# Optimization experiments

Measured on AMD Instinct MI355X. Metric: run time of the kernel, lower is better.

The kernel has to match this reference:

```python
import jax, jax.numpy as jnp
import numpy as np

EPS = 1e-6
NUM_HEADS = 16  # config.num_attention_heads

def _rms(h, w):
    h32 = h.astype(jnp.float32)
    v = jnp.mean(h32 * h32, axis=-1, keepdims=True)
    return (w * h32 * jax.lax.rsqrt(v + EPS)).astype(h.dtype)

def _rope(q, k, pos):
    dh = q.shape[-1]
    inv = 1.0 / (10000.0 ** (jnp.arange(0, dh, 2, dtype=jnp.float32) / dh))
    ang = pos.astype(jnp.float32)[:, None] * inv[None, :]  # [n, dh/2]
    cos = jnp.concatenate([jnp.cos(ang), jnp.cos(ang)], -1)[None, None]  # [1,1,n,dh]
    sin = jnp.concatenate([jnp.sin(ang), jnp.sin(ang)], -1)[None, None]
    def rot(x):
        x1, x2 = x[..., :dh // 2], x[..., dh // 2:]
        return jnp.concatenate([-x2, x1], -1)
    return q * cos + rot(q) * sin, k * cos + rot(k) * sin

def _skip_causal_mask(N, block_size, len1, text_len):
    qi = jnp.arange(N)[:, None]
    ki = jnp.arange(N)[None, :]
    qb = (qi - text_len) // block_size
    kb = (ki - text_len) // block_size
    iq = qi >= text_len
    ik = ki >= text_len
    return (((ki < text_len) & (qi >= ki))
            | (iq & ik & (qb < len1) & (kb < len1) & (qb >= kb))
            | (iq & ik & (qb >= len1) & (kb < len1) & (qb - len1 > kb))
            | (iq & ik & (qb == kb)))

def _layer(x, position_ids, text_position_ids, qkv_w, qkv_b, proj_w, proj_b,
           qn_w, kn_w, ln1_w, ln2_w, gate_w, up_w, down_w,
           block_size, text_len, len1):
    B, N, C = x.shape
    H = NUM_HEADS
    Dh = C // H
    T = text_len
    Lc = len1 * block_size
    offs = [0, T, T + Lc]
    lens = [T, Lc, N - T - Lc]  # text / clean / noised segment lengths
    qs, ks, vs = [], [], []
    for i in range(3):
        seg = _rms(x[:, offs[i]:offs[i] + lens[i]], ln1_w[i])  # input layernorm
        qkv = seg @ qkv_w[i] + qkv_b[i]                        # [B,n,3C]
        qkv = qkv.reshape(B, lens[i], 3, H, Dh).transpose(2, 0, 3, 1, 4)
        qs.append(_rms(qkv[0], qn_w[i]))
        ks.append(_rms(qkv[1], kn_w[i]))
        vs.append(qkv[2])
    img_q = jnp.concatenate([qs[1], qs[2]], axis=2)
    img_k = jnp.concatenate([ks[1], ks[2]], axis=2)
    img_q, img_k = _rope(img_q, img_k, position_ids)
    txt_q, txt_k = _rope(qs[0], ks[0], text_position_ids)
    q = jnp.concatenate([txt_q, img_q], axis=2)
    k = jnp.concatenate([txt_k, img_k], axis=2)
    v = jnp.concatenate(vs, axis=2)
    scores = jnp.einsum('bhqd,bhkd->bhqk', q, k) / np.float32(np.sqrt(Dh))
    mask = _skip_causal_mask(N, block_size, len1, text_len)
    scores = jnp.where(mask, scores, jnp.finfo(scores.dtype).min)
    attn = jax.nn.softmax(scores, axis=-1)
    o = jnp.einsum('bhqk,bhkd->bhqd', attn, v)
    o = o.transpose(0, 2, 1, 3).reshape(B, N, C)
    o = jnp.concatenate([o[:, offs[i]:offs[i] + lens[i]] @ proj_w[i] + proj_b[i]
                         for i in range(3)], axis=1)
    h = x + o
    mlp = []
    for i in range(3):
        y = _rms(h[:, offs[i]:offs[i] + lens[i]], ln2_w[i])  # post-attn layernorm
        mlp.append((jax.nn.silu(y @ gate_w[i]) * (y @ up_w[i])) @ down_w[i])
    return h + jnp.concatenate(mlp, axis=1)

def setup_inputs():
    key = jax.random.key(0)
    ks = jax.random.split(key, 8)
    B, C, H, I = 2, 1024, 16, 4096
    block_size, text_len, len1, len2 = 128, 256, 4, 4
    N = text_len + (len1 + len2) * block_size  # 1280
    s = 0.02
    return {
        'x': jax.random.normal(ks[0], (B, N, C), jnp.float32),
        'position_ids': jnp.arange((len1 + len2) * block_size, dtype=jnp.int32),
        'text_position_ids': jnp.arange(text_len, dtype=jnp.int32),
        'qkv_w': jax.random.normal(ks[1], (3, C, 3 * C), jnp.float32) * s,
        'qkv_b': jnp.zeros((3, 3 * C), jnp.float32),
        'proj_w': jax.random.normal(ks[2], (3, C, C), jnp.float32) * s,
        'proj_b': jnp.zeros((3, C), jnp.float32),
        'qn_w': jnp.ones((3, C // H), jnp.float32),
        'kn_w': jnp.ones((3, C // H), jnp.float32),
        'ln1_w': jnp.ones((3, C), jnp.float32),
        'ln2_w': jnp.ones((3, C), jnp.float32),
        'gate_w': jax.random.normal(ks[3], (3, C, I), jnp.float32) * s,
        'up_w': jax.random.normal(ks[4], (3, C, I), jnp.float32) * s,
        'down_w': jax.random.normal(ks[5], (3, I, C), jnp.float32) * s,
        'block_size': block_size, 'text_len': text_len, 'len1': len1,
    }

def reference(x, position_ids, text_position_ids, qkv_w, qkv_b, proj_w, proj_b,
              qn_w, kn_w, ln1_w, ln2_w, gate_w, up_w, down_w,
              block_size, text_len, len1):
    return _layer(x, position_ids, text_position_ids, qkv_w, qkv_b, proj_w, proj_b,
                  qn_w, kn_w, ln1_w, ln2_w, gate_w, up_w, down_w,
                  block_size, text_len, len1)
```

## Files before the change

kernel.cpp:

```cpp
#include <hip/hip_runtime.h>
#include <math.h>

constexpr int Bb  = 2;
constexpr int Nn  = 1280;
constexpr int Cc  = 1024;
constexpr int Hh  = 16;
constexpr int DH  = 64;
constexpr int Ii  = 4096;
constexpr int Tt  = 256;
constexpr int BSz = 128;
constexpr int L1  = 4;
constexpr int Mrows = Bb * Nn;

typedef __attribute__((ext_vector_type(8))) short short8v;
typedef __attribute__((ext_vector_type(4))) float f32x4;

__device__ __forceinline__ int segof(int n) {
    return n < Tt ? 0 : (n < Tt + L1 * BSz ? 1 : 2);
}
__device__ __forceinline__ unsigned short f2bf(float f) {
    unsigned int u = __float_as_uint(f);
    u += 0x7fffu + ((u >> 16) & 1u);
    return (unsigned short)(u >> 16);
}
__device__ __forceinline__ float bf2f(unsigned short h) {
    return __uint_as_float(((unsigned int)h) << 16);
}

__device__ __forceinline__ int xcd_swz(int lin, int nwg) {
    int cpx = nwg >> 3;
    return (lin & 7) * cpx + (lin >> 3);
}

__global__ __launch_bounds__(256)
void rms_bf16(const float* __restrict__ in, const float* __restrict__ w,
              unsigned short* __restrict__ out) {
    int row = blockIdx.x;
    int n   = row % Nn;
    int seg = segof(n);
    const float* x = in + (size_t)row * Cc;
    int t = threadIdx.x;
    float4 xv = reinterpret_cast<const float4*>(x)[t];
    float ss = xv.x * xv.x + xv.y * xv.y + xv.z * xv.z + xv.w * xv.w;
#pragma unroll
    for (int off = 32; off; off >>= 1) ss += __shfl_down(ss, off, 64);
    __shared__ float red[4];
    __shared__ float s_r;
    int lane = t & 63, wid = t >> 6;
    if (lane == 0) red[wid] = ss;
    __syncthreads();
    if (t == 0) s_r = rsqrtf((red[0] + red[1] + red[2] + red[3]) * (1.0f / Cc) + 1e-6f);
    __syncthreads();
    float r = s_r;
    float4 wv = reinterpret_cast<const float4*>(w + (size_t)seg * Cc)[t];
    ushort4 ov;
    ov.x = f2bf(wv.x * xv.x * r);
    ov.y = f2bf(wv.y * xv.y * r);
    ov.z = f2bf(wv.z * xv.z * r);
    ov.w = f2bf(wv.w * xv.w * r);
    *reinterpret_cast<ushort4*>(&out[(size_t)row * Cc + t * 4]) = ov;
}

__global__ __launch_bounds__(256)
void pack_w(const float* __restrict__ W, unsigned short* __restrict__ PB,
            int K, int Nd) {
    size_t idx = (size_t)blockIdx.x * 256 + threadIdx.x;
    size_t cpseg = (size_t)K * Nd / 8;
    int s = (int)(idx / cpseg);
    size_t rm = idx % cpseg;
    int lane = (int)(rm & 63);
    int fr   = (int)((rm >> 6) & 7);
    size_t tile = rm >> 9;
    int nct = Nd >> 7;
    int cb = (int)(tile % nct);
    int kt = (int)(tile / nct);
    int col = cb * 128 + fr * 16 + (lane & 15);
    int k0  = kt * 32 + (lane >> 4) * 8;
    const float* src = W + ((size_t)s * K + k0) * Nd + col;
    unsigned short o[8];
#pragma unroll
    for (int j = 0; j < 8; j++) o[j] = f2bf(src[(size_t)j * Nd]);
    short8v v;
#pragma unroll
    for (int j = 0; j < 8; j++) v[j] = (short)o[j];
    *reinterpret_cast<short8v*>(&PB[idx * 8]) = v;
}

template <int OUTMODE, bool BIAS, int NZ>
__global__ __launch_bounds__(256)
void gemm64(const unsigned short* __restrict__ A,
            const unsigned short* __restrict__ PB,
            const float* __restrict__ bias, void* __restrict__ outp,
            int K, int Nd) {
    __shared__ __align__(16) unsigned short lds[12288];
    int bx = blockIdx.x, by = blockIdx.y, bz = (NZ > 1) ? blockIdx.z : 0;
    {
        int gx = gridDim.x, gy = gridDim.y, gz = (NZ > 1) ? gridDim.z : 1;
        int lin = bx + gx * (by + gy * bz);
        int swz = xcd_swz(lin, gx * gy * gz);
        bx = swz % gx; swz /= gx;
        by = swz % gy; bz = swz / gy;
    }
    int rb = bx * 64, cb = by;
    int seg = segof(rb % Nn);
    int tid = threadIdx.x, lane = tid & 63, wid = tid >> 6;
    int wr = wid >> 1, wc = wid & 1;
    int g = lane >> 4, c_ = lane & 15;
    const unsigned short* PBseg = PB + (size_t)seg * K * Nd;
    const int nct = Nd >> 7;
    const int Keff = K / NZ;
    const int nKt = Keff >> 6;
    const int kz = bz * Keff;

    f32x4 acc[2][4];
#pragma unroll
    for (int m = 0; m < 2; m++)
#pragma unroll
        for (int n = 0; n < 4; n++) acc[m][n] = (f32x4){0.f, 0.f, 0.f, 0.f};

    short8v av[2], bv[4];
    auto load_tile = [&](int kt) {
#pragma unroll
        for (int i = 0; i < 2; i++) {
            int c = tid + i * 256;
            int rf = c >> 7, kb = (c >> 6) & 1, lc = c & 63;
            int row = rb + rf * 16 + (lc & 15);
            int k0  = kz + kt * 64 + kb * 32 + (lc >> 4) * 8;
            av[i] = *reinterpret_cast<const short8v*>(&A[(size_t)row * K + k0]);
        }
#pragma unroll
        for (int i = 0; i < 4; i++) {
            int c = tid + i * 256;
            int cf = c >> 7, kb = (c >> 6) & 1, lc = c & 63;
            int kt32 = (kz >> 5) + kt * 2 + kb;
            bv[i] = *reinterpret_cast<const short8v*>(
                &PBseg[((((size_t)kt32 * nct + cb) * 8 + cf) * 64 + lc) * 8]);
        }
    };

    load_tile(0);
    for (int kt = 0; kt < nKt; ++kt) {
        __syncthreads();
#pragma unroll
        for (int i = 0; i < 2; i++)
            *reinterpret_cast<short8v*>(&lds[(size_t)(tid + i * 256) * 8]) = av[i];
#pragma unroll
        for (int i = 0; i < 4; i++)
            *reinterpret_cast<short8v*>(&lds[4096 + (size_t)(tid + i * 256) * 8]) = bv[i];
        __syncthreads();
        if (kt + 1 < nKt) load_tile(kt + 1);
        short8v afr[2][2], bfr[4][2];
#pragma unroll
        for (int m = 0; m < 2; m++)
#pragma unroll
            for (int kb = 0; kb < 2; kb++)
                afr[m][kb] = *reinterpret_cast<short8v*>(
                    &lds[(((wr * 2 + m) * 2 + kb) * 64 + lane) * 8]);
#pragma unroll
        for (int n = 0; n < 4; n++)
#pragma unroll
            for (int kb = 0; kb < 2; kb++)
                bfr[n][kb] = *reinterpret_cast<short8v*>(
                    &lds[4096 + (((wc * 4 + n) * 2 + kb) * 64 + lane) * 8]);
#pragma unroll
        for (int m = 0; m < 2; m++)
#pragma unroll
            for (int n = 0; n < 4; n++)
#pragma unroll
                for (int kb = 0; kb < 2; kb++)
                    acc[m][n] = __builtin_amdgcn_mfma_f32_16x16x32_bf16(
                        afr[m][kb], bfr[n][kb], acc[m][n], 0, 0, 0);
    }

    float* outf = (float*)outp;
    unsigned short* outh = (unsigned short*)outp;
    size_t zoff = (NZ > 1) ? (size_t)bz * Mrows * Nd : 0;
#pragma unroll
    for (int n = 0; n < 4; n++) {
        int col = cb * 128 + wc * 64 + n * 16 + c_;
        float bvv = BIAS ? bias[(size_t)seg * Nd + col] : 0.f;
#pragma unroll
        for (int m = 0; m < 2; m++) {
#pragma unroll
            for (int r = 0; r < 4; r++) {
                int row = rb + wr * 32 + m * 16 + g * 4 + r;
                float v = acc[m][n][r] + bvv;
                if (OUTMODE == 0) outf[zoff + (size_t)row * Nd + col] = v;
                else              outh[zoff + (size_t)row * Nd + col] = f2bf(v);
            }
        }
    }
}

__global__ __launch_bounds__(256)
void gemm_gu(const unsigned short* __restrict__ A,
             const unsigned short* __restrict__ PG,
             const unsigned short* __restrict__ PU,
             unsigned short* __restrict__ outp) {
    __shared__ __align__(16) unsigned short lds[10240];
    int bx = blockIdx.x, by = blockIdx.y;
    {
        int lin = bx + gridDim.x * by;
        int swz = xcd_swz(lin, gridDim.x * gridDim.y);
        bx = swz % gridDim.x; by = swz / gridDim.x;
    }
    int rb = bx * 64, cb = by;
    int seg = segof(rb % Nn);
    int tid = threadIdx.x, lane = tid & 63, wid = tid >> 6;
    int wr = wid >> 1, wc = wid & 1;
    int g = lane >> 4, c_ = lane & 15;
    const int nct = Ii >> 7;
    const unsigned short* PGseg = PG + (size_t)seg * Cc * Ii;
    const unsigned short* PUseg = PU + (size_t)seg * Cc * Ii;

    f32x4 accG[2][4], accU[2][4];
#pragma unroll
    for (int m = 0; m < 2; m++)
#pragma unroll
        for (int n = 0; n < 4; n++) {
            accG[m][n] = (f32x4){0.f, 0.f, 0.f, 0.f};
            accU[m][n] = (f32x4){0.f, 0.f, 0.f, 0.f};
        }

    int mf0 = tid >> 6, lc0 = tid & 63;
    const unsigned short* gA =
        &A[(size_t)(rb + mf0 * 16 + (lc0 & 15)) * Cc + (lc0 >> 4) * 8];
    const size_t bstep = (size_t)nct * 4096;
    short8v av, gv[2], uv[2];
    auto load_tile = [&](int kt) {
        av = *reinterpret_cast<const short8v*>(gA + kt * 32);
#pragma unroll
        for (int i = 0; i < 2; i++) {
            int c = tid + i * 256;
            int cf = c >> 6, lc = c & 63;
            size_t off = (((size_t)kt * nct + cb) * 8 + cf) * 64 * 8 + (size_t)lc * 8;
            gv[i] = *reinterpret_cast<const short8v*>(PGseg + off);
            uv[i] = *reinterpret_cast<const short8v*>(PUseg + off);
        }
    };

    const int nKt = Cc >> 5;
    load_tile(0);
    for (int kt = 0; kt < nKt; ++kt) {
        __syncthreads();
        *reinterpret_cast<short8v*>(&lds[(size_t)tid * 8]) = av;
#pragma unroll
        for (int i = 0; i < 2; i++) {
            *reinterpret_cast<short8v*>(&lds[2048 + (size_t)(tid + i * 256) * 8]) = gv[i];
            *reinterpret_cast<short8v*>(&lds[6144 + (size_t)(tid + i * 256) * 8]) = uv[i];
        }
        __syncthreads();
        if (kt + 1 < nKt) load_tile(kt + 1);
        short8v afr[2], gfr[4], ufr[4];
#pragma unroll
        for (int m = 0; m < 2; m++)
            afr[m] = *reinterpret_cast<short8v*>(&lds[((wr * 2 + m) * 64 + lane) * 8]);
#pragma unroll
        for (int n = 0; n < 4; n++) {
            gfr[n] = *reinterpret_cast<short8v*>(&lds[2048 + ((wc * 4 + n) * 64 + lane) * 8]);
            ufr[n] = *reinterpret_cast<short8v*>(&lds[6144 + ((wc * 4 + n) * 64 + lane) * 8]);
        }
#pragma unroll
        for (int m = 0; m < 2; m++)
#pragma unroll
            for (int n = 0; n < 4; n++) {
                accG[m][n] = __builtin_amdgcn_mfma_f32_16x16x32_bf16(
                    afr[m], gfr[n], accG[m][n], 0, 0, 0);
                accU[m][n] = __builtin_amdgcn_mfma_f32_16x16x32_bf16(
                    afr[m], ufr[n], accU[m][n], 0, 0, 0);
            }
    }

#pragma unroll
    for (int n = 0; n < 4; n++) {
        int col = cb * 128 + wc * 64 + n * 16 + c_;
#pragma unroll
        for (int m = 0; m < 2; m++) {
#pragma unroll
            for (int r = 0; r < 4; r++) {
                int row = rb + wr * 32 + m * 16 + g * 4 + r;
                float gval = accG[m][n][r], uval = accU[m][n][r];
                float t = gval / (1.f + __expf(-gval)) * uval;
                outp[(size_t)row * Ii + col] = f2bf(t);
            }
        }
    }
}

__global__ __launch_bounds__(256)
void combine_proj(const float* __restrict__ x, const float* __restrict__ bias,
                  const float* __restrict__ p, float* __restrict__ hb) {
    int i = blockIdx.x * 256 + threadIdx.x;
    int base = i * 4;
    int col = base % Cc;
    int n   = (base / Cc) % Nn;
    int seg = segof(n);
    float4 a = reinterpret_cast<const float4*>(x)[i];
    float4 b = *reinterpret_cast<const float4*>(&bias[(size_t)seg * Cc + col]);
    float4 p0 = reinterpret_cast<const float4*>(p)[i];
    float4 p1 = reinterpret_cast<const float4*>(p)[i + Mrows * Cc / 4];
    float4 r;
    r.x = a.x + b.x + p0.x + p1.x;
    r.y = a.y + b.y + p0.y + p1.y;
    r.z = a.z + b.z + p0.z + p1.z;
    r.w = a.w + b.w + p0.w + p1.w;
    reinterpret_cast<float4*>(hb)[i] = r;
}

__global__ __launch_bounds__(256)
void combine_down4(const unsigned short* __restrict__ p,
                   float* __restrict__ out) {
    int i = blockIdx.x * 256 + threadIdx.x;
    float4 a = reinterpret_cast<const float4*>(out)[i];
#pragma unroll
    for (int z = 0; z < 4; z++) {
        ushort4 u = *reinterpret_cast<const ushort4*>(&p[(size_t)z * Mrows * Cc + i * 4]);
        a.x += bf2f(u.x); a.y += bf2f(u.y); a.z += bf2f(u.z); a.w += bf2f(u.w);
    }
    reinterpret_cast<float4*>(out)[i] = a;
}

__global__ __launch_bounds__(256)
void split_rope(const unsigned short* __restrict__ qkv,
                const float* __restrict__ qn_w, const float* __restrict__ kn_w,
                const int* __restrict__ pos_ids, const int* __restrict__ tpos_ids,
                unsigned short* __restrict__ Q, unsigned short* __restrict__ K,
                unsigned short* __restrict__ V) {
    int row = blockIdx.x;
    int b = row / Nn, n = row % Nn;
    int seg = segof(n);
    int lane = threadIdx.x & 63, wid = threadIdx.x >> 6;
    int pos = (n < Tt) ? tpos_ids[n] : pos_ids[n - Tt];
    int j = lane & 31;
    float ang = (float)pos * exp2f(-(float)j * (13.287712379549449f / 32.f));
    float cv = cosf(ang), sv = sinf(ang);
    float qw = qn_w[seg * DH + lane], kw = kn_w[seg * DH + lane];
    for (int h = wid; h < Hh; h += 4) {
        const unsigned short* base = qkv + (size_t)row * (3 * Cc) + h * DH + lane;
        float q = bf2f(base[0]), k = bf2f(base[Cc]), v = bf2f(base[2 * Cc]);
        float qs = q * q, ks = k * k;
#pragma unroll
        for (int off = 32; off; off >>= 1) {
            qs += __shfl_xor(qs, off, 64);
            ks += __shfl_xor(ks, off, 64);
        }
        q = q * rsqrtf(qs * (1.f / DH) + 1e-6f) * qw;
        k = k * rsqrtf(ks * (1.f / DH) + 1e-6f) * kw;
        float qp = __shfl_xor(q, 32, 64);
        float kp = __shfl_xor(k, 32, 64);
        float qo = q * cv + ((lane < 32) ? -qp * sv : qp * sv);
        float ko = k * cv + ((lane < 32) ? -kp * sv : kp * sv);
        size_t oidx = ((size_t)(b * Hh + h) * Nn + n) * DH + lane;
        Q[oidx] = f2bf(qo);
        K[oidx] = f2bf(ko);
        V[oidx] = f2bf(v);
    }
}

__global__ __launch_bounds__(256)
void attn_mfma(const unsigned short* __restrict__ Qg,
               const unsigned short* __restrict__ Kg,
               const unsigned short* __restrict__ Vg,
               unsigned short* __restrict__ O) {
    __shared__ __align__(16) unsigned short k_lds[64 * 64];
    __shared__ __align__(16) unsigned short vt_lds[64 * 64];
    __shared__ __align__(16) unsigned short p_lds[4][16 * 64];

    int qt = blockIdx.x;
    int bh = blockIdx.y;
    int b = bh >> 4, h = bh & 15;
    int tid = threadIdx.x, lane = tid & 63, wid = tid >> 6;
    int g = lane >> 4, c = lane & 15;

    const size_t headoff = (size_t)bh * Nn * DH;
    int q0 = qt * 64;
    bool qtext = q0 < Tt;
    int qb = qtext ? 0 : (q0 - Tt) / BSz;

    int qrow_frag = q0 + wid * 16 + c;
    short8v aq[2];
#pragma unroll
    for (int kb = 0; kb < 2; kb++)
        aq[kb] = *reinterpret_cast<const short8v*>(
            &Qg[headoff + (size_t)qrow_frag * DH + kb * 32 + g * 8]);

    unsigned short* pbuf = &p_lds[wid][0];

    f32x4 o_[4];
#pragma unroll
    for (int nb = 0; nb < 4; nb++) o_[nb] = (f32x4){0.f, 0.f, 0.f, 0.f};
    float m_[4] = {-3.4e38f, -3.4e38f, -3.4e38f, -3.4e38f};
    float l_[4] = {0.f, 0.f, 0.f, 0.f};

    int tr = tid >> 2, tc = tid & 3;

    for (int kt = 0; kt < Nn / 64; kt++) {
        int kbase = kt * 64;
        bool vis, diag = false;
        if (qtext) {
            vis = (kbase <= q0);
            diag = (kbase == q0);
        } else if (kbase < Tt) {
            vis = true;
        } else {
            int kb = (kbase - Tt) / BSz;
            vis = (qb < L1) ? (kb <= qb)
                            : ((kb < L1 && qb - L1 > kb) || kb == qb);
        }
        if (!vis) continue;

        __syncthreads();
        {
            const unsigned short* ks = &Kg[headoff + (size_t)(kbase + tr) * DH];
            const unsigned short* vs = &Vg[headoff + (size_t)(kbase + tr) * DH];
#pragma unroll
            for (int i = 0; i < 2; i++) {
                int ch = tc + i * 4;
                short8v kv = *reinterpret_cast<const short8v*>(ks + ch * 8);
                int byte = (tr * 128 + ch * 16) ^ ((tr & 7) << 4);
                *reinterpret_cast<short8v*>((char*)k_lds + byte) = kv;
                short8v vv = *reinterpret_cast<const short8v*>(vs + ch * 8);
#pragma unroll
                for (int j = 0; j < 8; j++) {
                    int dh = ch * 8 + j;
                    int vbyte = (dh * 128 + tr * 2) ^ ((dh & 7) << 4);
                    *reinterpret_cast<unsigned short*>((char*)vt_lds + vbyte) =
                        (unsigned short)vv[j];
                }
            }
        }
        __syncthreads();

        f32x4 s_[4];
#pragma unroll
        for (int nb = 0; nb < 4; nb++) s_[nb] = (f32x4){0.f, 0.f, 0.f, 0.f};
#pragma unroll
        for (int nb = 0; nb < 4; nb++) {
            int kil = nb * 16 + c;
#pragma unroll
            for (int kb = 0; kb < 2; kb++) {
                int byte = (kil * 128 + kb * 64 + g * 16) ^ ((kil & 7) << 4);
                short8v bk = *reinterpret_cast<short8v*>((char*)k_lds + byte);
                s_[nb] = __builtin_amdgcn_mfma_f32_16x16x32_bf16(aq[kb], bk, s_[nb], 0, 0, 0);
            }
        }
#pragma unroll
        for (int nb = 0; nb < 4; nb++) {
#pragma unroll
            for (int r = 0; r < 4; r++) {
                float sv = s_[nb][r] * 0.125f;
                if (diag) {
                    int qrl = wid * 16 + g * 4 + r;
                    int kcl = nb * 16 + c;
                    if (qrl < kcl) sv = -3.4e38f;
                }
                s_[nb][r] = sv;
            }
        }
#pragma unroll
        for (int r = 0; r < 4; r++) {
            float mx = fmaxf(fmaxf(s_[0][r], s_[1][r]), fmaxf(s_[2][r], s_[3][r]));
#pragma unroll
            for (int off = 1; off <= 8; off <<= 1)
                mx = fmaxf(mx, __shfl_xor(mx, off, 64));
            float mn = fmaxf(m_[r], mx);
            float es = __expf(m_[r] - mn);
            m_[r] = mn;
            float pv[4];
            float rs = 0.f;
#pragma unroll
            for (int nb = 0; nb < 4; nb++) {
                pv[nb] = __expf(s_[nb][r] - mn);
                rs += pv[nb];
            }
#pragma unroll
            for (int off = 1; off <= 8; off <<= 1)
                rs += __shfl_xor(rs, off, 64);
            l_[r] = l_[r] * es + rs;
#pragma unroll
            for (int nb = 0; nb < 4; nb++) o_[nb][r] *= es;
            int qrl = g * 4 + r;
            int swz = (qrl & 7) << 4;
#pragma unroll
            for (int nb = 0; nb < 4; nb++) {
                int byte = (qrl * 128 + (nb * 16 + c) * 2) ^ swz;
                *reinterpret_cast<unsigned short*>((char*)pbuf + byte) = f2bf(pv[nb]);
            }
        }
        short8v aP[2];
#pragma unroll
        for (int kb = 0; kb < 2; kb++) {
            int byte = (c * 128 + kb * 64 + g * 16) ^ ((c & 7) << 4);
            aP[kb] = *reinterpret_cast<short8v*>((char*)pbuf + byte);
        }
#pragma unroll
        for (int nb = 0; nb < 4; nb++) {
            int dh = nb * 16 + c;
#pragma unroll
            for (int kb = 0; kb < 2; kb++) {
                int byte = (dh * 128 + kb * 64 + g * 16) ^ ((dh & 7) << 4);
                short8v bv = *reinterpret_cast<short8v*>((char*)vt_lds + byte);
                o_[nb] = __builtin_amdgcn_mfma_f32_16x16x32_bf16(aP[kb], bv, o_[nb], 0, 0, 0);
            }
        }
    }

    float inv_[4];
#pragma unroll
    for (int r = 0; r < 4; r++) inv_[r] = 1.f / l_[r];
#pragma unroll
    for (int nb = 0; nb < 4; nb++) {
        int col = h * DH + nb * 16 + c;
#pragma unroll
        for (int r = 0; r < 4; r++) {
            int row = q0 + wid * 16 + g * 4 + r;
            O[((size_t)b * Nn + row) * Cc + col] = f2bf(o_[nb][r] * inv_[r]);
        }
    }
}

extern "C" void kernel_launch(void* const* d_in, const int* in_sizes, int n_in,
                              void* d_out, int out_size, void* d_ws, size_t ws_size,
                              hipStream_t stream) {
    const float* x        = (const float*)d_in[0];
    const int*   pos_ids  = (const int*)d_in[1];
    const int*   tpos_ids = (const int*)d_in[2];
    const float* qkv_w    = (const float*)d_in[3];
    const float* qkv_b    = (const float*)d_in[4];
    const float* proj_w   = (const float*)d_in[5];
    const float* proj_b   = (const float*)d_in[6];
    const float* qn_w     = (const float*)d_in[7];
    const float* kn_w     = (const float*)d_in[8];
    const float* ln1_w    = (const float*)d_in[9];
    const float* ln2_w    = (const float*)d_in[10];
    const float* gate_w   = (const float*)d_in[11];
    const float* up_w     = (const float*)d_in[12];
    const float* down_w   = (const float*)d_in[13];
    float* out = (float*)d_out;
    char*  wsb = (char*)d_ws;

    unsigned short* WA  = (unsigned short*)(wsb);
    unsigned short* WB  = (unsigned short*)(wsb + 25165824);
    unsigned short* Tb  = (unsigned short*)(wsb + 50331648);
    unsigned short* P3  = (unsigned short*)(wsb + 71303168);
    unsigned short* Qbf = Tb;
    unsigned short* Kbf = Tb + 2621440;
    unsigned short* Vbf = Tb + 5242880;

    rms_bf16<<<Mrows, 256, 0, stream>>>(x, ln1_w, P3);
    pack_w<<<4608, 256, 0, stream>>>(qkv_w, WA, Cc, 3 * Cc);
    gemm64<1, true, 1><<<dim3(Mrows / 64, 24), 256, 0, stream>>>(
        P3, WA, qkv_b, WB, Cc, 3 * Cc);
    split_rope<<<Mrows, 256, 0, stream>>>(WB, qn_w, kn_w, pos_ids, tpos_ids,
                                          Qbf, Kbf, Vbf);
    attn_mfma<<<dim3(Nn / 64, Bb * Hh), 256, 0, stream>>>(Qbf, Kbf, Vbf, P3);
    pack_w<<<1536, 256, 0, stream>>>(proj_w, WA, Cc, Cc);
    gemm64<0, false, 2><<<dim3(Mrows / 64, 8, 2), 256, 0, stream>>>(
        P3, WA, nullptr, (float*)Tb, Cc, Cc);
    combine_proj<<<Mrows * Cc / 1024, 256, 0, stream>>>(x, proj_b, (float*)Tb, out);
    rms_bf16<<<Mrows, 256, 0, stream>>>(out, ln2_w, P3);
    pack_w<<<6144, 256, 0, stream>>>(gate_w, WA, Cc, Ii);
    pack_w<<<6144, 256, 0, stream>>>(up_w, WB, Cc, Ii);
    gemm_gu<<<dim3(Mrows / 64, 32), 256, 0, stream>>>(P3, WA, WB, Tb);
    pack_w<<<6144, 256, 0, stream>>>(down_w, WA, Ii, Cc);
    gemm64<1, false, 4><<<dim3(Mrows / 64, 8, 4), 256, 0, stream>>>(
        Tb, WA, nullptr, WB, Ii, Cc);
    combine_down4<<<Mrows * Cc / 1024, 256, 0, stream>>>(WB, out);
}
```

Before: 287.1 us.

## Enlarge GEMM block tiles to 128x128 with 32-wide K steps

Measured after the change: 275.2 us. 4.1% less time.

```diff
diff --git a/kernel.cpp b/kernel.cpp
--- a/kernel.cpp
+++ b/kernel.cpp
@@ -87,12 +87,12 @@
 }
 
 template <int OUTMODE, bool BIAS, int NZ>
-__global__ __launch_bounds__(256)
-void gemm64(const unsigned short* __restrict__ A,
-            const unsigned short* __restrict__ PB,
-            const float* __restrict__ bias, void* __restrict__ outp,
-            int K, int Nd) {
-    __shared__ __align__(16) unsigned short lds[12288];
+__global__ __launch_bounds__(256, 2)
+void gemm128r(const unsigned short* __restrict__ A,
+              const unsigned short* __restrict__ PB,
+              const float* __restrict__ bias, void* __restrict__ outp,
+              int K, int Nd) {
+    __shared__ __align__(16) unsigned short lds[8192];
     int bx = blockIdx.x, by = blockIdx.y, bz = (NZ > 1) ? blockIdx.z : 0;
     {
         int gx = gridDim.x, gy = gridDim.y, gz = (NZ > 1) ? gridDim.z : 1;
@@ -101,75 +101,66 @@
         bx = swz % gx; swz /= gx;
         by = swz % gy; bz = swz / gy;
     }
-    int rb = bx * 64, cb = by;
+    int rb = bx * 128, cb = by;
     int seg = segof(rb % Nn);
     int tid = threadIdx.x, lane = tid & 63, wid = tid >> 6;
     int wr = wid >> 1, wc = wid & 1;
     int g = lane >> 4, c_ = lane & 15;
-    const unsigned short* PBseg = PB + (size_t)seg * K * Nd;
     const int nct = Nd >> 7;
     const int Keff = K / NZ;
-    const int nKt = Keff >> 6;
+    const int nKt = Keff >> 5;
     const int kz = bz * Keff;
-
-    f32x4 acc[2][4];
-#pragma unroll
-    for (int m = 0; m < 2; m++)
+    const unsigned short* PBseg = PB + (size_t)seg * K * Nd;
+
+    int mf0 = tid >> 6, lc0 = tid & 63;
+    const unsigned short* pA0 =
+        A + (size_t)(rb + mf0 * 16 + (lc0 & 15)) * K + kz + (lc0 >> 4) * 8;
+    const unsigned short* pA1 = pA0 + (size_t)64 * K;
+    const unsigned short* pB0 =
+        PBseg + (((size_t)(kz >> 5) * nct + cb) * 8 + mf0) * 512 + (size_t)lc0 * 8;
+    const unsigned short* pB1 = pB0 + 2048;
+    const size_t bstep = (size_t)nct * 4096;
+
+    f32x4 acc[4][4];
+#pragma unroll
+    for (int m = 0; m < 4; m++)
 #pragma unroll
         for (int n = 0; n < 4; n++) acc[m][n] = (f32x4){0.f, 0.f, 0.f, 0.f};
 
-    short8v av[2], bv[4];
-    auto load_tile = [&](int kt) {
-#pragma unroll
-        for (int i = 0; i < 2; i++) {
-            int c = tid + i * 256;
-            int rf = c >> 7, kb = (c >> 6) & 1, lc = c & 63;
-            int row = rb + rf * 16 + (lc & 15);
-            int k0  = kz + kt * 64 + kb * 32 + (lc >> 4) * 8;
-            av[i] = *reinterpret_cast<const short8v*>(&A[(size_t)row * K + k0]);
-        }
-#pragma unroll
-        for (int i = 0; i < 4; i++) {
-            int c = tid + i * 256;
-            int cf = c >> 7, kb = (c >> 6) & 1, lc = c & 63;
-            int kt32 = (kz >> 5) + kt * 2 + kb;
-            bv[i] = *reinterpret_cast<const short8v*>(
-                &PBseg[((((size_t)kt32 * nct + cb) * 8 + cf) * 64 + lc) * 8]);
-        }
-    };
-
-    load_tile(0);
+    short8v av[2], bv[2];
+    av[0] = *reinterpret_cast<const short8v*>(pA0);
+    av[1] = *reinterpret_cast<const short8v*>(pA1);
+    bv[0] = *reinterpret_cast<const short8v*>(pB0);
+    bv[1] = *reinterpret_cast<const short8v*>(pB1);
+    pA0 += 32; pA1 += 32; pB0 += bstep; pB1 += bstep;
+
     for (int kt = 0; kt < nKt; ++kt) {
         __syncthreads();
-#pragma unroll
-        for (int i = 0; i < 2; i++)
-            *reinterpret_cast<short8v*>(&lds[(size_t)(tid + i * 256) * 8]) = av[i];
-#pragma unroll
-        for (int i = 0; i < 4; i++)
-            *reinterpret_cast<short8v*>(&lds[4096 + (size_t)(tid + i * 256) * 8]) = bv[i];
+        *reinterpret_cast<short8v*>(&lds[(size_t)tid * 8]) = av[0];
+        *reinterpret_cast<short8v*>(&lds[(size_t)(tid + 256) * 8]) = av[1];
+        *reinterpret_cast<short8v*>(&lds[4096 + (size_t)tid * 8]) = bv[0];
+        *reinterpret_cast<short8v*>(&lds[4096 + (size_t)(tid + 256) * 8]) = bv[1];
         __syncthreads();
-        if (kt + 1 < nKt) load_tile(kt + 1);
-        short8v afr[2][2], bfr[4][2];
-#pragma unroll
-        for (int m = 0; m < 2; m++)
-#pragma unroll
-            for (int kb = 0; kb < 2; kb++)
-                afr[m][kb] = *reinterpret_cast<short8v*>(
-                    &lds[(((wr * 2 + m) * 2 + kb) * 64 + lane) * 8]);
+        if (kt + 1 < nKt) {
+            av[0] = *reinterpret_cast<const short8v*>(pA0);
+            av[1] = *reinterpret_cast<const short8v*>(pA1);
+            bv[0] = *reinterpret_cast<const short8v*>(pB0);
+            bv[1] = *reinterpret_cast<const short8v*>(pB1);
+            pA0 += 32; pA1 += 32; pB0 += bstep; pB1 += bstep;
+        }
+        short8v afr[4], bfr[4];
+#pragma unroll
+        for (int m = 0; m < 4; m++)
+            afr[m] = *reinterpret_cast<short8v*>(&lds[((wr * 4 + m) * 64 + lane) * 8]);
 #pragma unroll
         for (int n = 0; n < 4; n++)
-#pragma unroll
-            for (int kb = 0; kb < 2; kb++)
-                bfr[n][kb] = *reinterpret_cast<short8v*>(
-                    &lds[4096 + (((wc * 4 + n) * 2 + kb) * 64 + lane) * 8]);
-#pragma unroll
-        for (int m = 0; m < 2; m++)
+            bfr[n] = *reinterpret_cast<short8v*>(&lds[4096 + ((wc * 4 + n) * 64 + lane) * 8]);
+#pragma unroll
+        for (int m = 0; m < 4; m++)
 #pragma unroll
             for (int n = 0; n < 4; n++)
-#pragma unroll
-                for (int kb = 0; kb < 2; kb++)
-                    acc[m][n] = __builtin_amdgcn_mfma_f32_16x16x32_bf16(
-                        afr[m][kb], bfr[n][kb], acc[m][n], 0, 0, 0);
+                acc[m][n] = __builtin_amdgcn_mfma_f32_16x16x32_bf16(
+                    afr[m], bfr[n], acc[m][n], 0, 0, 0);
     }
 
     float* outf = (float*)outp;
@@ -180,10 +171,10 @@
         int col = cb * 128 + wc * 64 + n * 16 + c_;
         float bvv = BIAS ? bias[(size_t)seg * Nd + col] : 0.f;
 #pragma unroll
-        for (int m = 0; m < 2; m++) {
+        for (int m = 0; m < 4; m++) {
 #pragma unroll
             for (int r = 0; r < 4; r++) {
-                int row = rb + wr * 32 + m * 16 + g * 4 + r;
+                int row = rb + wr * 64 + m * 16 + g * 4 + r;
                 float v = acc[m][n][r] + bvv;
                 if (OUTMODE == 0) outf[zoff + (size_t)row * Nd + col] = v;
                 else              outh[zoff + (size_t)row * Nd + col] = f2bf(v);
@@ -192,19 +183,19 @@
     }
 }
 
-__global__ __launch_bounds__(256)
+__global__ __launch_bounds__(256, 2)
 void gemm_gu(const unsigned short* __restrict__ A,
              const unsigned short* __restrict__ PG,
              const unsigned short* __restrict__ PU,
              unsigned short* __restrict__ outp) {
-    __shared__ __align__(16) unsigned short lds[10240];
+    __shared__ __align__(16) unsigned short lds[12288];
     int bx = blockIdx.x, by = blockIdx.y;
     {
         int lin = bx + gridDim.x * by;
         int swz = xcd_swz(lin, gridDim.x * gridDim.y);
         bx = swz % gridDim.x; by = swz / gridDim.x;
     }
-    int rb = bx * 64, cb = by;
+    int rb = bx * 128, cb = by;
     int seg = segof(rb % Nn);
     int tid = threadIdx.x, lane = tid & 63, wid = tid >> 6;
     int wr = wid >> 1, wc = wid & 1;
@@ -213,72 +204,92 @@
     const unsigned short* PGseg = PG + (size_t)seg * Cc * Ii;
     const unsigned short* PUseg = PU + (size_t)seg * Cc * Ii;
 
-    f32x4 accG[2][4], accU[2][4];
-#pragma unroll
-    for (int m = 0; m < 2; m++)
+    int mf0 = tid >> 6, lc0 = tid & 63;
+    const unsigned short* pA0 =
+        A + (size_t)(rb + mf0 * 16 + (lc0 & 15)) * Cc + (lc0 >> 4) * 8;
+    const unsigned short* pA1 = pA0 + (size_t)64 * Cc;
+    size_t boff = ((size_t)cb * 8 + mf0) * 512 + (size_t)lc0 * 8;
+    const unsigned short* pG0 = PGseg + boff;
+    const unsigned short* pG1 = pG0 + 2048;
+    const unsigned short* pU0 = PUseg + boff;
+    const unsigned short* pU1 = pU0 + 2048;
+    const size_t bstep = (size_t)nct * 4096;
+
+    f32x4 accG[4][4], accU[4][4];
+#pragma unroll
+    for (int m = 0; m < 4; m++)
 #pragma unroll
         for (int n = 0; n < 4; n++) {
             accG[m][n] = (f32x4){0.f, 0.f, 0.f, 0.f};
             accU[m][n] = (f32x4){0.f, 0.f, 0.f, 0.f};
         }
 
-    int mf0 = tid >> 6, lc0 = tid & 63;
-    const unsigned short* gA =
-        &A[(size_t)(rb + mf0 * 16 + (lc0 & 15)) * Cc + (lc0 >> 4) * 8];
-    const size_t bstep = (size_t)nct * 4096;
-    short8v av, gv[2], uv[2];
-    auto load_tile = [&](int kt) {
-        av = *reinterpret_cast<const short8v*>(gA + kt * 32);
-#pragma unroll
-        for (int i = 0; i < 2; i++) {
-            int c = tid + i * 256;
-            int cf = c >> 6, lc = c & 63;
-            size_t off = (((size_t)kt * nct + cb) * 8 + cf) * 64 * 8 + (size_t)lc * 8;
-            gv[i] = *reinterpret_cast<const short8v*>(PGseg + off);
-            uv[i] = *reinterpret_cast<const short8v*>(PUseg + off);
-        }
-    };
+    short8v av[2], gv[2], uv[2];
+    av[0] = *reinterpret_cast<const short8v*>(pA0);
+    av[1] = *reinterpret_cast<const short8v*>(pA1);
+    gv[0] = *reinterpret_cast<const short8v*>(pG0);
+    gv[1] = *reinterpret_cast<const short8v*>(pG1);
+    uv[0] = *reinterpret_cast<const short8v*>(pU0);
+    uv[1] = *reinterpret_cast<const short8v*>(pU1);
+    pA0 += 32; pA1 += 32; pG0 += bstep; pG1 += bstep; pU0 += bstep; pU1 += bstep;
 
     const int nKt = Cc >> 5;
-    load_tile(0);
     for (int kt = 0; kt < nKt; ++kt) {
         __syncthreads();
-        *reinterpret_cast<short8v*>(&lds[(size_t)tid * 8]) = av;
-#pragma unroll
-        for (int i = 0; i < 2; i++) {
-            *reinterpret_cast<short8v*>(&lds[2048 + (size_t)(tid + i * 256) * 8]) = gv[i];
-            *reinterpret_cast<short8v*>(&lds[6144 + (size_t)(tid + i * 256) * 8]) = uv[i];
-        }
+        *reinterpret_cast<short8v*>(&lds[(size_t)tid * 8]) = av[0];
+        *reinterpret_cast<short8v*>(&lds[(size_t)(tid + 256) * 8]) = av[1];
+        *reinterpret_cast<short8v*>(&lds[4096 + (size_t)tid * 8]) = gv[0];
+        *reinterpret_cast<short8v*>(&lds[4096 + (size_t)(tid + 256) * 8]) = gv[1];
+        *reinterpret_cast<short8v*>(&lds[8192 + (size_t)tid * 8]) = uv[0];
+        *reinterpret_cast<short8v*>(&lds[8192 + (size_t)(tid + 256) * 8]) = uv[1];
         __syncthreads();
-        if (kt + 1 < nKt) load_tile(kt + 1);
-        short8v afr[2], gfr[4], ufr[4];
-#pragma unroll
-        for (int m = 0; m < 2; m++)
-            afr[m] = *reinterpret_cast<short8v*>(&lds[((wr * 2 + m) * 64 + lane) * 8]);
-#pragma unroll
-        for (int n = 0; n < 4; n++) {
-            gfr[n] = *reinterpret_cast<short8v*>(&lds[2048 + ((wc * 4 + n) * 64 + lane) * 8]);
-            ufr[n] = *reinterpret_cast<short8v*>(&lds[6144 + ((wc * 4 + n) * 64 + lane) * 8]);
-        }
-#pragma unroll
-        for (int m = 0; m < 2; m++)
-#pragma unroll
-            for (int n = 0; n < 4; n++) {
-                accG[m][n] = __builtin_amdgcn_mfma_f32_16x16x32_bf16(
-                    afr[m], gfr[n], accG[m][n], 0, 0, 0);
-                accU[m][n] = __builtin_amdgcn_mfma_f32_16x16x32_bf16(
-                    afr[m], ufr[n], accU[m][n], 0, 0, 0);
-            }
+        if (kt + 1 < nKt) {
+            av[0] = *reinterpret_cast<const short8v*>(pA0);
+            av[1] = *reinterpret_cast<const short8v*>(pA1);
+            gv[0] = *reinterpret_cast<const short8v*>(pG0);
+            gv[1] = *reinterpret_cast<const short8v*>(pG1);
+            uv[0] = *reinterpret_cast<const short8v*>(pU0);
+            uv[1] = *reinterpret_cast<const short8v*>(pU1);
+            pA0 += 32; pA1 += 32; pG0 += bstep; pG1 += bstep; pU0 += bstep; pU1 += bstep;
+        }
+        short8v afr[4];
+#pragma unroll
+        for (int m = 0; m < 4; m++)
+            afr[m] = *reinterpret_cast<short8v*>(&lds[((wr * 4 + m) * 64 + lane) * 8]);
+        {
+            short8v gfr[4];
+#pragma unroll
+            for (int n = 0; n < 4; n++)
+                gfr[n] = *reinterpret_cast<short8v*>(&lds[4096 + ((wc * 4 + n) * 64 + lane) * 8]);
+#pragma unroll
+            for (int m = 0; m < 4; m++)
+#pragma unroll
+                for (int n = 0; n < 4; n++)
+                    accG[m][n] = __builtin_amdgcn_mfma_f32_16x16x32_bf16(
+                        afr[m], gfr[n], accG[m][n], 0, 0, 0);
+        }
+        {
+            short8v ufr[4];
+#pragma unroll
+            for (int n = 0; n < 4; n++)
+                ufr[n] = *reinterpret_cast<short8v*>(&lds[8192 + ((wc * 4 + n) * 64 + lane) * 8]);
+#pragma unroll
+            for (int m = 0; m < 4; m++)
+#pragma unroll
+                for (int n = 0; n < 4; n++)
+                    accU[m][n] = __builtin_amdgcn_mfma_f32_16x16x32_bf16(
+                        afr[m], ufr[n], accU[m][n], 0, 0, 0);
+        }
     }
 
 #pragma unroll
     for (int n = 0; n < 4; n++) {
         int col = cb * 128 + wc * 64 + n * 16 + c_;
 #pragma unroll
-        for (int m = 0; m < 2; m++) {
+        for (int m = 0; m < 4; m++) {
 #pragma unroll
             for (int r = 0; r < 4; r++) {
-                int row = rb + wr * 32 + m * 16 + g * 4 + r;
+                int row = rb + wr * 64 + m * 16 + g * 4 + r;
                 float gval = accG[m][n][r], uval = accU[m][n][r];
                 float t = gval / (1.f + __expf(-gval)) * uval;
                 outp[(size_t)row * Ii + col] = f2bf(t);
@@ -549,21 +560,21 @@
 
     rms_bf16<<<Mrows, 256, 0, stream>>>(x, ln1_w, P3);
     pack_w<<<4608, 256, 0, stream>>>(qkv_w, WA, Cc, 3 * Cc);
-    gemm64<1, true, 1><<<dim3(Mrows / 64, 24), 256, 0, stream>>>(
+    gemm128r<1, true, 1><<<dim3(Mrows / 128, 24), 256, 0, stream>>>(
         P3, WA, qkv_b, WB, Cc, 3 * Cc);
     split_rope<<<Mrows, 256, 0, stream>>>(WB, qn_w, kn_w, pos_ids, tpos_ids,
                                           Qbf, Kbf, Vbf);
     attn_mfma<<<dim3(Nn / 64, Bb * Hh), 256, 0, stream>>>(Qbf, Kbf, Vbf, P3);
     pack_w<<<1536, 256, 0, stream>>>(proj_w, WA, Cc, Cc);
-    gemm64<0, false, 2><<<dim3(Mrows / 64, 8, 2), 256, 0, stream>>>(
+    gemm128r<0, false, 2><<<dim3(Mrows / 128, 8, 2), 256, 0, stream>>>(
         P3, WA, nullptr, (float*)Tb, Cc, Cc);
     combine_proj<<<Mrows * Cc / 1024, 256, 0, stream>>>(x, proj_b, (float*)Tb, out);
     rms_bf16<<<Mrows, 256, 0, stream>>>(out, ln2_w, P3);
     pack_w<<<6144, 256, 0, stream>>>(gate_w, WA, Cc, Ii);
     pack_w<<<6144, 256, 0, stream>>>(up_w, WB, Cc, Ii);
-    gemm_gu<<<dim3(Mrows / 64, 32), 256, 0, stream>>>(P3, WA, WB, Tb);
+    gemm_gu<<<dim3(Mrows / 128, 32), 256, 0, stream>>>(P3, WA, WB, Tb);
     pack_w<<<6144, 256, 0, stream>>>(down_w, WA, Ii, Cc);
-    gemm64<1, false, 4><<<dim3(Mrows / 64, 8, 4), 256, 0, stream>>>(
+    gemm128r<1, false, 4><<<dim3(Mrows / 128, 8, 4), 256, 0, stream>>>(
         Tb, WA, nullptr, WB, Ii, Cc);
     combine_down4<<<Mrows * Cc / 1024, 256, 0, stream>>>(WB, out);
 }
```
